# Performance work log

Hardware: AMD Instinct MI355X
Metric: run time of the kernel (lower is better)

## Reference

```python
import jax, jax.numpy as jnp
import numpy as np

B = 2
D = 256
NH = 8
DH = D // NH
L = 4
K = 2                       # sampling grid per box side
NP = K * K                  # sampled points per level
FF = 1024
NQ = 300
NE = 6
ND = 6
REF_SIZE = 4.0
SHAPES = ((64, 64), (32, 32), (16, 16), (8, 8))
S = sum(h * w for h, w in SHAPES)


def make_ref_windows():
    ws = []
    for (H, W) in SHAPES:
        y = (jnp.arange(1, H + 1, dtype=jnp.float32) - 0.5) / (H + 1e-6)
        x = (jnp.arange(1, W + 1, dtype=jnp.float32) - 0.5) / (W + 1e-6)
        yy, xx = jnp.meshgrid(y, x, indexing='ij')
        ctr = jnp.stack([xx, yy], -1).reshape(-1, 2)
        size = jnp.broadcast_to(jnp.array([REF_SIZE / W, REF_SIZE / H], jnp.float32), ctr.shape)
        ws.append(jnp.concatenate([ctr, size], -1))
    return jnp.broadcast_to(jnp.concatenate(ws, 0)[None], (B, S, 4))


def layernorm(x, g, b):
    m = jnp.mean(x, -1, keepdims=True)
    v = jnp.mean((x - m) ** 2, -1, keepdims=True)
    return (x - m) / jnp.sqrt(v + 1e-5) * g + b


def inverse_sigmoid(x, eps=1e-5):
    x = jnp.clip(x, eps, 1.0 - eps)
    return jnp.log(x / (1.0 - x))


def bilinear_sample(vl, pts, Hl, Wl):
    # vl: [B, Hl*Wl, NH, DH], pts: [B, N, NP, 2] normalized to [0,1]
    x = pts[..., 0] * Wl - 0.5
    y = pts[..., 1] * Hl - 0.5
    x0f = jnp.floor(x); y0f = jnp.floor(y)
    wx = x - x0f; wy = y - y0f
    x0 = x0f.astype(jnp.int32); y0 = y0f.astype(jnp.int32)
    Bn, N, P = x.shape

    def gather(yi, xi):
        valid = ((xi >= 0) & (xi < Wl) & (yi >= 0) & (yi < Hl)).astype(vl.dtype)
        idx = jnp.clip(yi, 0, Hl - 1) * Wl + jnp.clip(xi, 0, Wl - 1)
        g = jnp.take_along_axis(vl, idx.reshape(Bn, N * P, 1, 1), axis=1)
        return g.reshape(Bn, N, P, NH, DH) * valid[..., None, None]

    w00 = ((1 - wx) * (1 - wy))[..., None, None]
    w01 = (wx * (1 - wy))[..., None, None]
    w10 = ((1 - wx) * wy)[..., None, None]
    w11 = (wx * wy)[..., None, None]
    return (gather(y0, x0) * w00 + gather(y0, x0 + 1) * w01
            + gather(y0 + 1, x0) * w10 + gather(y0 + 1, x0 + 1) * w11)


def box_attention(q, memory, ref_windows, Wv, bv, Wa, ba, Wo, bo):
    # q: [B,N,D], memory: [B,S,D], ref_windows: [B,N,4] (cx,cy,w,h)
    Bn, N, _ = q.shape
    v = (memory @ Wv + bv).reshape(Bn, memory.shape[1], NH, DH)
    attn = jax.nn.softmax((q @ Wa + ba).reshape(Bn, N, NH, L * NP), axis=-1)
    g = (jnp.arange(K, dtype=jnp.float32) + 0.5) / K - 0.5   # grid fractions in box
    gy, gx = jnp.meshgrid(g, g, indexing='ij')
    grid = jnp.stack([gx.ravel(), gy.ravel()], -1)           # [NP,2]
    pts = ref_windows[:, :, None, :2] + grid[None, None] * ref_windows[:, :, None, 2:]
    out = jnp.zeros((Bn, N, NH, DH), q.dtype)
    start = 0
    for l, (Hl, Wl) in enumerate(SHAPES):
        sl = Hl * Wl
        sampled = bilinear_sample(v[:, start:start + sl], pts, Hl, Wl)  # [B,N,NP,NH,DH]
        out = out + jnp.einsum('bnphd,bnhp->bnhd', sampled, attn[..., l * NP:(l + 1) * NP])
        start += sl
    return out.reshape(Bn, N, D) @ Wo + bo


def mha(q_in, k_in, v_in, Wqkv, bqkv, Wo, bo):
    Bn, N, _ = q_in.shape
    q = (q_in @ Wqkv[:, :D] + bqkv[:D]).reshape(Bn, N, NH, DH)
    k = (k_in @ Wqkv[:, D:2 * D] + bqkv[D:2 * D]).reshape(Bn, N, NH, DH)
    v = (v_in @ Wqkv[:, 2 * D:] + bqkv[2 * D:]).reshape(Bn, N, NH, DH)
    a = jax.nn.softmax(jnp.einsum('bqhd,bkhd->bhqk', q, k) / jnp.sqrt(jnp.float32(DH)), axis=-1)
    o = jnp.einsum('bhqk,bkhd->bqhd', a, v).reshape(Bn, N, D)
    return o @ Wo + bo


def pos_embed_2d(coords):
    # coords: [B,N,2] -> [B,N,D] sine embedding (deformable-DETR style)
    npf = D // 2
    dim_t = 10000.0 ** (2.0 * (jnp.arange(npf) // 2) / npf)
    p = coords[..., None] * (2 * np.pi) / dim_t               # [B,N,2,npf]
    p = jnp.stack([jnp.sin(p[..., 0::2]), jnp.cos(p[..., 1::2])], -1)
    return p.reshape(coords.shape[0], coords.shape[1], 2 * npf)


def reference(src, pos, eWv, ebv, eWa, eba, eWo, ebo, eW1, eb1, eW2, eb2,
              en1g, en1b, en2g, en2b,
              dWqkv, dbqkv, dWso, dbso, dWv, dbv, dWa, dba, dWo, dbo,
              dW1, db1, dW2, db2, dn1g, dn1b, dn2g, dn2b, dn3g, dn3b,
              cls_w, cls_b, bb_w1, bb_b1, bb_w2, bb_b2, bb_w3, bb_b3,
              el_w, el_b, el_g, el_beta):
    ref_windows = make_ref_windows()
    out = src
    for i in range(NE):
        a = box_attention(out + pos, out, ref_windows, eWv[i], ebv[i], eWa[i], eba[i], eWo[i], ebo[i])
        out = layernorm(out + a, en1g[i], en1b[i])
        f = jax.nn.relu(out @ eW1[i] + eb1[i]) @ eW2[i] + eb2[i]
        out = layernorm(out + f, en2g[i], en2b[i])
    # proposal selection (topk + gather)
    valid = jnp.all((ref_windows[..., :2] > 0.01) & (ref_windows[..., :2] < 0.99), axis=-1)
    logits = (out @ cls_w + cls_b)[..., 0]
    logits = jnp.where(valid, logits, -65504.0)
    _, idx = jax.lax.top_k(logits, NQ)
    q_emb = jnp.take_along_axis(out, idx[..., None], axis=1)
    tgt = layernorm(jax.lax.stop_gradient(q_emb) @ el_w + el_b, el_g, el_beta)
    ref_sel = jnp.take_along_axis(ref_windows, idx[..., None], axis=1)
    h = jax.nn.relu(q_emb @ bb_w1 + bb_b1)
    h = jax.nn.relu(h @ bb_w2 + bb_b2)
    tmp = h @ bb_w3 + bb_b3 + inverse_sigmoid(ref_sel)
    out_ref = jax.lax.stop_gradient(jax.nn.sigmoid(tmp))
    query_pos = pos_embed_2d(out_ref[..., :2]) + pos_embed_2d(out_ref[..., 2:])
    # decoder
    x = tgt
    inter = []
    for i in range(ND):
        qk = x + query_pos
        sa = mha(qk, qk, x, dWqkv[i], dbqkv[i], dWso[i], dbso[i])
        x = layernorm(x + sa, dn1g[i], dn1b[i])
        ca = box_attention(x + query_pos, out, out_ref, dWv[i], dbv[i], dWa[i], dba[i], dWo[i], dbo[i])
        x = layernorm(x + ca, dn2g[i], dn2b[i])
        f = jax.nn.relu(x @ dW1[i] + db1[i]) @ dW2[i] + db2[i]
        x = layernorm(x + f, dn3g[i], dn3b[i])
        inter.append(x)
    return jnp.stack(inter)  # [ND, B, NQ, D]


def setup_inputs() -> dict:
    key = jax.random.key(0)
    kit = iter(jax.random.split(key, 80))
    def rn(shape, s=0.02):
        return jax.random.normal(next(kit), shape, jnp.float32) * s
    z = lambda *sh: jnp.zeros(sh, jnp.float32)
    o = lambda *sh: jnp.ones(sh, jnp.float32)
    A = NH * L * NP
    return dict(
        src=jax.random.normal(next(kit), (B, S, D), jnp.float32),
        pos=jax.random.normal(next(kit), (B, S, D), jnp.float32),
        eWv=rn((NE, D, D)), ebv=z(NE, D), eWa=rn((NE, D, A)), eba=z(NE, A),
        eWo=rn((NE, D, D)), ebo=z(NE, D),
        eW1=rn((NE, D, FF)), eb1=z(NE, FF), eW2=rn((NE, FF, D)), eb2=z(NE, D),
        en1g=o(NE, D), en1b=z(NE, D), en2g=o(NE, D), en2b=z(NE, D),
        dWqkv=rn((ND, D, 3 * D)), dbqkv=z(ND, 3 * D),
        dWso=rn((ND, D, D)), dbso=z(ND, D),
        dWv=rn((ND, D, D)), dbv=z(ND, D), dWa=rn((ND, D, A)), dba=z(ND, A),
        dWo=rn((ND, D, D)), dbo=z(ND, D),
        dW1=rn((ND, D, FF)), db1=z(ND, FF), dW2=rn((ND, FF, D)), db2=z(ND, D),
        dn1g=o(ND, D), dn1b=z(ND, D), dn2g=o(ND, D), dn2b=z(ND, D), dn3g=o(ND, D), dn3b=z(ND, D),
        cls_w=rn((D, 1)), cls_b=z(1),
        bb_w1=rn((D, D)), bb_b1=z(D), bb_w2=rn((D, D)), bb_b2=z(D),
        bb_w3=rn((D, 4)), bb_b3=z(4),
        el_w=rn((D, D)), el_b=z(D), el_g=o(D), el_beta=z(D),
    )
```

## Files before the change

### kernel.cpp

```cpp
#include <hip/hip_runtime.h>
#include <hip/hip_bf16.h>
#include <math.h>

typedef unsigned short u16;
typedef unsigned int u32;
typedef unsigned long long u64;

#define Bc   2
#define NHc  8
#define Sc   5440
#define NQc  300
#define NEc  6
#define NDc  6
#define FFc  1024
#define BSc  (Bc*Sc)
#define BNQc (Bc*NQc)

__device__ __forceinline__ float us2f(u16 u) {
    union { float f; unsigned v; } x; x.v = ((unsigned)u) << 16; return x.f;
}

__device__ __forceinline__ u16 f2bf(float f) {
    unsigned u = __float_as_uint(f);
    unsigned r = u + 0x7FFFu + ((u >> 16) & 1u);
    return (u16)(r >> 16);
}
__device__ __forceinline__ float bf2f(u16 u) { return us2f(u); }
__device__ __forceinline__ unsigned pk2(u16 a, u16 b) { return (unsigned)a | ((unsigned)b << 16); }

__device__ __forceinline__ size_t pidx(int row, int k) {
    return (size_t)(k >> 5) * ((size_t)BSc * 32) + ((size_t)row << 5) + (size_t)(k & 31);
}

__device__ __forceinline__ int xcd_swz(int orig, int nwg) {
    int xcd = orig & 7;
    int q = nwg >> 3, r = nwg & 7;
    int base = (xcd < r) ? xcd * (q + 1) : r * (q + 1) + (xcd - r) * q;
    return base + (orig >> 3);
}

using bf16x8 = __attribute__((ext_vector_type(8))) short;
using f32x4  = __attribute__((ext_vector_type(4))) float;

__global__ void k_detect(const u16* __restrict__ src, int* __restrict__ flag) {
    __shared__ int cnt;
    if (threadIdx.x == 0) cnt = 0;
    __syncthreads();
    u16 v = src[threadIdx.x];
    int e = (v >> 7) & 0xFF;
    int plaus = (e == 0) || (e >= 107 && e <= 131);
    atomicAdd(&cnt, plaus);
    __syncthreads();
    if (threadIdx.x == 0) *flag = (cnt >= 224) ? 1 : 0;
}

struct CvtArgs {
    const void* in[48];
    long off[48];
    int n[48];
    int cnt;
    long total;
};
__global__ void k_cvt_all8(CvtArgs args, float* __restrict__ out,
                           const int* __restrict__ flag) {
    long g = ((long)blockIdx.x * 256 + threadIdx.x) * 8;
    if (g >= args.total) return;
    int lo = 0, hi = args.cnt - 1;
    while (lo < hi) {
        int mid = (lo + hi + 1) >> 1;
        if (args.off[mid] <= g) lo = mid; else hi = mid - 1;
    }
    long local = g - args.off[lo];
    long n = (long)args.n[lo];
    float v[8];
#pragma unroll
    for (int j = 0; j < 8; ++j) v[j] = 0.f;
    if (*flag) {
        const u16* p = (const u16*)args.in[lo] + local;
        if (local + 8 <= n) {
            uint4 r = *(const uint4*)p;
            const u16* pu = (const u16*)&r;
#pragma unroll
            for (int j = 0; j < 8; ++j) v[j] = us2f(pu[j]);
        } else {
            for (int j = 0; j < 8; ++j)
                if (local + j < n) v[j] = us2f(p[j]);
        }
    } else {
        const float* p = (const float*)args.in[lo] + local;
        if (local + 8 <= n) {
            float4 a = ((const float4*)p)[0];
            float4 b = ((const float4*)p)[1];
            v[0] = a.x; v[1] = a.y; v[2] = a.z; v[3] = a.w;
            v[4] = b.x; v[5] = b.y; v[6] = b.z; v[7] = b.w;
        } else {
            for (int j = 0; j < 8; ++j)
                if (local + j < n) v[j] = p[j];
        }
    }
    float4 o0, o1;
    o0.x = v[0]; o0.y = v[1]; o0.z = v[2]; o0.w = v[3];
    o1.x = v[4]; o1.y = v[5]; o1.z = v[6]; o1.w = v[7];
    ((float4*)(out + g))[0] = o0;
    ((float4*)(out + g))[1] = o1;
}

__global__ void k_addf2(const float* __restrict__ a, const float* __restrict__ pos,
                        u16* __restrict__ ah, u16* __restrict__ al,
                        u16* __restrict__ ph, u16* __restrict__ pl, int n) {
    int i = blockIdx.x * 256 + threadIdx.x;
    if (i >= n) return;
    int row = i >> 8, k = i & 255;
    size_t px = pidx(row, k);
    float x = a[i];
    u16 h = f2bf(x);
    ah[px] = h;
    al[px] = f2bf(x - bf2f(h));
    float s = x + pos[i];
    u16 h2 = f2bf(s);
    ph[px] = h2;
    pl[px] = f2bf(s - bf2f(h2));
}

template<int RELU>
__global__ __launch_bounds__(256) void k_mgemm(
    const u16* __restrict__ Ah, const u16* __restrict__ Al,
    const float* __restrict__ W, const u16* __restrict__ Wraw, int ldw,
    const float* __restrict__ bias,
    float* __restrict__ C, u16* __restrict__ Ch, u16* __restrict__ Cl,
    int ldc, int K,
    const int* __restrict__ flag) {
    __shared__ __align__(16) u16 lsAH[4096];
    __shared__ __align__(16) u16 lsAL[4096];
    __shared__ __align__(16) u16 lsBH[4096];
    __shared__ __align__(16) u16 lsBL[4096];
    const int t = threadIdx.x;
    int lin = blockIdx.x + gridDim.x * blockIdx.y;
    lin = xcd_swz(lin, gridDim.x * gridDim.y);
    const int row0 = (lin / gridDim.x) * 128, col0 = (lin % gridDim.x) * 128;
    const int fast = *flag;
    const size_t PSLAB = (size_t)BSc * 32;

    const int c0 = t, c1 = 256 + t;
    const size_t abase = (size_t)row0 * 32;
    const u16* a0h = Ah + abase + (size_t)c0 * 8;
    const u16* a1h = Ah + abase + (size_t)c1 * 8;
    const u16* a0l = Al + abase + (size_t)c0 * 8;
    const u16* a1l = Al + abase + (size_t)c1 * 8;
    const unsigned d0 = (((unsigned)c0 & ~3u) | (((unsigned)c0 & 3u) ^ (((unsigned)c0 >> 3) & 3u))) * 8u;
    const unsigned d1 = (((unsigned)c1 & ~3u) | (((unsigned)c1 & 3u) ^ (((unsigned)c1 >> 3) & 3u))) * 8u;

    const int bkp = t >> 4, bno = t & 15;
    const float* bp = W + (size_t)(bkp * 2) * ldw + col0 + bno * 8;
    const u16*  brp = Wraw + (size_t)(bkp * 2) * ldw + col0 + bno * 8;

    const int lane = t & 63;
    const int w = t >> 6;
    const int wr = (w >> 1) * 64, wc = (w & 1) * 64;
    const int kg = lane >> 4, lr = lane & 15;

    unsigned iaf[4];
#pragma unroll
    for (int mi = 0; mi < 4; ++mi) {
        int arow = wr + mi * 16 + lr;
        iaf[mi] = ((unsigned)(arow << 2) + ((unsigned)kg ^ (((unsigned)arow >> 1) & 3u))) * 8u;
    }

    f32x4 acc[4][4] = {};
    uint4 aU0h, aU1h, aU0l, aU1l;
    float4 bR[4];
    uint4 bU0, bU1;
    aU0h = *(const uint4*)a0h;
    aU1h = *(const uint4*)a1h;
    aU0l = *(const uint4*)a0l;
    aU1l = *(const uint4*)a1l;
    if (fast) {
        bU0 = *(const uint4*)brp;
        bU1 = *(const uint4*)(brp + ldw);
    } else {
        const float4* q0 = (const float4*)bp;
        const float4* q1 = (const float4*)(bp + ldw);
        bR[0] = q0[0]; bR[1] = q0[1]; bR[2] = q1[0]; bR[3] = q1[1];
    }

    for (int k0 = 0; k0 < K; k0 += 32) {
        if (k0) __syncthreads();
        *(uint4*)&lsAH[d0] = aU0h;
        *(uint4*)&lsAH[d1] = aU1h;
        *(uint4*)&lsAL[d0] = aU0l;
        *(uint4*)&lsAL[d1] = aU1l;
        {
            unsigned bb = (unsigned)(bkp >> 2) * 1024u + (unsigned)(bkp & 3) * 2u;
            if (fast) {
                const u16* e0 = (const u16*)&bU0;
                const u16* e1 = (const u16*)&bU1;
#pragma unroll
                for (int j = 0; j < 8; ++j) {
                    int slot = bno * 8 + (j ^ (bno & 7));
                    *(unsigned*)&lsBH[bb + (unsigned)slot * 8u] = pk2(e0[j], e1[j]);
                }
            } else {
                float e0f[8], e1f[8];
                *(float4*)&e0f[0] = bR[0]; *(float4*)&e0f[4] = bR[1];
                *(float4*)&e1f[0] = bR[2]; *(float4*)&e1f[4] = bR[3];
#pragma unroll
                for (int j = 0; j < 8; ++j) {
                    int slot = bno * 8 + (j ^ (bno & 7));
                    u16 h0 = f2bf(e0f[j]), h1 = f2bf(e1f[j]);
                    *(unsigned*)&lsBH[bb + (unsigned)slot * 8u] = pk2(h0, h1);
                    u16 l0 = f2bf(e0f[j] - bf2f(h0));
                    u16 l1 = f2bf(e1f[j] - bf2f(h1));
                    *(unsigned*)&lsBL[bb + (unsigned)slot * 8u] = pk2(l0, l1);
                }
            }
        }
        __syncthreads();
        if (k0 + 32 < K) {
            size_t soff = (size_t)((k0 >> 5) + 1) * PSLAB;
            aU0h = *(const uint4*)(a0h + soff);
            aU1h = *(const uint4*)(a1h + soff);
            aU0l = *(const uint4*)(a0l + soff);
            aU1l = *(const uint4*)(a1l + soff);
            if (fast) {
                bU0 = *(const uint4*)(brp + (size_t)(k0 + 32) * ldw);
                bU1 = *(const uint4*)(brp + (size_t)(k0 + 33) * ldw);
            } else {
                const float4* q0 = (const float4*)(bp + (size_t)(k0 + 32) * ldw);
                const float4* q1 = (const float4*)(bp + (size_t)(k0 + 33) * ldw);
                bR[0] = q0[0]; bR[1] = q0[1]; bR[2] = q1[0]; bR[3] = q1[1];
            }
        }
        bf16x8 aH[4], aL[4], bH[4], bL[4];
#pragma unroll
        for (int mi = 0; mi < 4; ++mi) {
            aH[mi] = *(const bf16x8*)&lsAH[iaf[mi]];
            aL[mi] = *(const bf16x8*)&lsAL[iaf[mi]];
        }
#pragma unroll
        for (int ni = 0; ni < 4; ++ni) {
            int c = wc + ni * 16 + lr;
            int slot = (c & ~7) | ((c ^ (c >> 3)) & 7);
            unsigned ib = (unsigned)kg * 1024u + (unsigned)slot * 8u;
            bH[ni] = *(const bf16x8*)&lsBH[ib];
            if (!fast) bL[ni] = *(const bf16x8*)&lsBL[ib];
        }
#pragma unroll
        for (int mi = 0; mi < 4; ++mi)
#pragma unroll
            for (int ni = 0; ni < 4; ++ni) {
                acc[mi][ni] = __builtin_amdgcn_mfma_f32_16x16x32_bf16(aH[mi], bH[ni], acc[mi][ni], 0, 0, 0);
                acc[mi][ni] = __builtin_amdgcn_mfma_f32_16x16x32_bf16(aL[mi], bH[ni], acc[mi][ni], 0, 0, 0);
            }
        if (!fast) {
#pragma unroll
            for (int mi = 0; mi < 4; ++mi)
#pragma unroll
                for (int ni = 0; ni < 4; ++ni)
                    acc[mi][ni] = __builtin_amdgcn_mfma_f32_16x16x32_bf16(aH[mi], bL[ni], acc[mi][ni], 0, 0, 0);
        }
    }
    const int rb = row0 + wr + (lane >> 4) * 4;
#pragma unroll
    for (int ni = 0; ni < 4; ++ni) {
        int cc = col0 + wc + ni * 16 + lr;
        float bv = bias[cc];
#pragma unroll
        for (int mi = 0; mi < 4; ++mi) {
#pragma unroll
            for (int r2 = 0; r2 < 4; ++r2) {
                int rr = rb + mi * 16 + r2;
                float v = acc[mi][ni][r2] + bv;
                if (RELU) v = fmaxf(v, 0.f);
                if (C) C[(size_t)rr * ldc + cc] = v;
                if (Ch) {
                    size_t px = pidx(rr, cc);
                    u16 h = f2bf(v);
                    Ch[px] = h;
                    Cl[px] = f2bf(v - bf2f(h));
                }
            }
        }
    }
}

template<int RELU>
__global__ __launch_bounds__(256) void k_dgemm(
    const float* __restrict__ A, int lda,
    const float* __restrict__ W, int ldw, int wcol0,
    const float* __restrict__ bias,
    float* __restrict__ C, int ldc,
    int M, int N, int K) {
    __shared__ float As[2][16][68];
    __shared__ float Bs[2][16][68];
    int t = threadIdx.x;
    int row0 = blockIdx.y * 64, col0 = blockIdx.x * 64;
    int ti = t >> 4, tj = t & 15;
    int arow = t >> 2, akq = (t & 3) << 2;
    int bk = t >> 4, bn = (t & 15) << 2;
    bool aok = (row0 + arow) < M;
    const float* ap = A + (size_t)(row0 + arow) * lda + akq;
    const float* bp = W + (size_t)bk * ldw + wcol0 + col0 + bn;
    float4 aR = aok ? *(const float4*)ap : make_float4(0.f, 0.f, 0.f, 0.f);
    float4 bR = *(const float4*)bp;
    As[0][akq + 0][arow] = aR.x;
    As[0][akq + 1][arow] = aR.y;
    As[0][akq + 2][arow] = aR.z;
    As[0][akq + 3][arow] = aR.w;
    *(float4*)&Bs[0][bk][bn] = bR;
    __syncthreads();
    int cur = 0;
    float acc[4][4] = {};
    for (int k0 = 0; k0 < K; k0 += 16) {
        bool more = (k0 + 16) < K;
        if (more) {
            aR = aok ? *(const float4*)(ap + k0 + 16) : make_float4(0.f, 0.f, 0.f, 0.f);
            bR = *(const float4*)(bp + (size_t)(k0 + 16) * ldw);
        }
#pragma unroll
        for (int k = 0; k < 16; ++k) {
            float a[4], b[4];
#pragma unroll
            for (int r = 0; r < 4; ++r) a[r] = As[cur][k][ti * 4 + r];
#pragma unroll
            for (int c = 0; c < 4; ++c) b[c] = Bs[cur][k][tj * 4 + c];
#pragma unroll
            for (int r = 0; r < 4; ++r)
#pragma unroll
                for (int c = 0; c < 4; ++c) acc[r][c] += a[r] * b[c];
        }
        if (more) {
            int nxt = cur ^ 1;
            As[nxt][akq + 0][arow] = aR.x;
            As[nxt][akq + 1][arow] = aR.y;
            As[nxt][akq + 2][arow] = aR.z;
            As[nxt][akq + 3][arow] = aR.w;
            *(float4*)&Bs[nxt][bk][bn] = bR;
            __syncthreads();
            cur = nxt;
        }
    }
    for (int r = 0; r < 4; ++r) {
        int rr = row0 + ti * 4 + r;
        if (rr >= M) continue;
        for (int c = 0; c < 4; ++c) {
            int cc = col0 + tj * 4 + c;
            float v = acc[r][c] + bias[cc];
            if (RELU) v = fmaxf(v, 0.f);
            C[(size_t)rr * ldc + cc] = v;
        }
    }
}

__global__ __launch_bounds__(256) void k_gemm4(
    const float* __restrict__ A, const float* __restrict__ W,
    const float* __restrict__ bias, const float* __restrict__ rsel,
    float* __restrict__ oref, int M, int K) {
    int row = blockIdx.x * 64 + (threadIdx.x >> 2);
    int col = threadIdx.x & 3;
    if (row >= M) return;
    float acc = 0.f;
    const float* a = A + (size_t)row * K;
    for (int k = 0; k < K; ++k) acc += a[k] * W[k * 4 + col];
    float tmp = acc + bias[col];
    float r = rsel[(size_t)row * 4 + col];
    r = fminf(fmaxf(r, 1e-5f), 1.f - 1e-5f);
    float v = tmp + logf(r / (1.f - r));
    oref[(size_t)row * 4 + col] = 1.f / (1.f + __expf(-v));
}

__global__ void k_ln(const float* __restrict__ a, const float* __restrict__ b,
                     const float* __restrict__ g, const float* __restrict__ be,
                     float* __restrict__ o,
                     u16* __restrict__ oh, u16* __restrict__ ol,
                     const float* __restrict__ padd, float* __restrict__ opadd,
                     u16* __restrict__ oph, u16* __restrict__ opl,
                     void* __restrict__ sdst, size_t soff,
                     const int* __restrict__ flag) {
    int row = blockIdx.x;
    int t = threadIdx.x;
    __shared__ float red[256];
    size_t ix = (size_t)row * 256 + t;
    float x = a[ix];
    if (b) x += b[ix];
    red[t] = x;
    __syncthreads();
    for (int s = 128; s > 0; s >>= 1) { if (t < s) red[t] += red[t + s]; __syncthreads(); }
    float mean = red[0] / 256.f;
    __syncthreads();
    float d = x - mean;
    red[t] = d * d;
    __syncthreads();
    for (int s = 128; s > 0; s >>= 1) { if (t < s) red[t] += red[t + s]; __syncthreads(); }
    float var = red[0] / 256.f;
    float y = d * rsqrtf(var + 1e-5f) * g[t] + be[t];
    o[ix] = y;
    if (oh) {
        size_t px = pidx(row, t);
        u16 h = f2bf(y);
        oh[px] = h;
        ol[px] = f2bf(y - bf2f(h));
    }
    if (padd) {
        float z = y + padd[ix];
        if (opadd) opadd[ix] = z;
        if (oph) {
            size_t px = pidx(row, t);
            u16 h = f2bf(z);
            oph[px] = h;
            opl[px] = f2bf(z - bf2f(h));
        }
    }
    if (sdst) {
        if (*flag) ((__hip_bfloat16*)sdst)[soff + ix] = __float2bfloat16(y);
        else       ((float*)sdst)[soff + ix] = y;
    }
}

__global__ void k_refw(float* __restrict__ rw) {
    int s = blockIdx.x * 256 + threadIdx.x;
    if (s >= Sc) return;
    int start, HW;
    if (s < 4096)      { start = 0;    HW = 64; }
    else if (s < 5120) { start = 4096; HW = 32; }
    else if (s < 5376) { start = 5120; HW = 16; }
    else               { start = 5376; HW = 8;  }
    int loc = s - start;
    int i = loc / HW, j = loc % HW;
    rw[s * 4 + 0] = (j + 0.5f) / ((float)HW + 1e-6f);
    rw[s * 4 + 1] = (i + 0.5f) / ((float)HW + 1e-6f);
    rw[s * 4 + 2] = 4.0f / (float)HW;
    rw[s * 4 + 3] = 4.0f / (float)HW;
}

__global__ __launch_bounds__(256) void k_box_sample4(
    const float* __restrict__ v, const float* __restrict__ attn,
    const float* __restrict__ refw, int ref_bs,
    float* __restrict__ out, u16* __restrict__ outh, u16* __restrict__ outl,
    int N) {
    const int t = threadIdx.x;
    const int qi = t >> 6, lane = t & 63;
    const int blk = xcd_swz(blockIdx.x, gridDim.x);
    const int n = blk * 4 + qi;
    const int b = blockIdx.y;
    if (n >= N) return;
    const float* arow = attn + ((size_t)b * N + n) * 128;
    float2 wl = *(const float2*)(arow + lane * 2);
    float m = fmaxf(wl.x, wl.y);
#pragma unroll
    for (int d2 = 1; d2 < 8; d2 <<= 1) m = fmaxf(m, __shfl_xor(m, d2, 8));
    float e0 = __expf(wl.x - m), e1 = __expf(wl.y - m);
    float s = e0 + e1;
#pragma unroll
    for (int d2 = 1; d2 < 8; d2 <<= 1) s += __shfl_xor(s, d2, 8);
    float inv = 1.f / s;
    e0 *= inv; e1 *= inv;

    const float* rw = refw + (size_t)ref_bs * b + (size_t)n * 4;
    float cx = rw[0], cy = rw[1], bw = rw[2], bh = rw[3];
    const float* vb = v + (size_t)b * Sc * 256 + lane * 4;
    float4 acc = make_float4(0.f, 0.f, 0.f, 0.f);
    int start = 0;
    const int HWs[4] = {64, 32, 16, 8};
#pragma unroll
    for (int l = 0; l < 4; ++l) {
        int HW = HWs[l];
#pragma unroll
        for (int p = 0; p < 4; ++p) {
            float gx = (p & 1) ? 0.25f : -0.25f;
            float gy = (p >> 1) ? 0.25f : -0.25f;
            float x = (cx + gx * bw) * (float)HW - 0.5f;
            float y = (cy + gy * bh) * (float)HW - 0.5f;
            float x0f = floorf(x), y0f = floorf(y);
            float wx = x - x0f, wy = y - y0f;
            int x0 = (int)x0f, y0 = (int)y0f;
            float4 smp = make_float4(0.f, 0.f, 0.f, 0.f);
            if (x0 >= 0 && x0 < HW && y0 >= 0 && y0 < HW) {
                float4 g4 = *(const float4*)(vb + (size_t)(start + y0 * HW + x0) * 256);
                float wgt = (1.f - wx) * (1.f - wy);
                smp.x += wgt * g4.x; smp.y += wgt * g4.y; smp.z += wgt * g4.z; smp.w += wgt * g4.w;
            }
            if (x0 + 1 >= 0 && x0 + 1 < HW && y0 >= 0 && y0 < HW) {
                float4 g4 = *(const float4*)(vb + (size_t)(start + y0 * HW + x0 + 1) * 256);
                float wgt = wx * (1.f - wy);
                smp.x += wgt * g4.x; smp.y += wgt * g4.y; smp.z += wgt * g4.z; smp.w += wgt * g4.w;
            }
            if (x0 >= 0 && x0 < HW && y0 + 1 >= 0 && y0 + 1 < HW) {
                float4 g4 = *(const float4*)(vb + (size_t)(start + (y0 + 1) * HW + x0) * 256);
                float wgt = (1.f - wx) * wy;
                smp.x += wgt * g4.x; smp.y += wgt * g4.y; smp.z += wgt * g4.z; smp.w += wgt * g4.w;
            }
            if (x0 + 1 >= 0 && x0 + 1 < HW && y0 + 1 >= 0 && y0 + 1 < HW) {
                float4 g4 = *(const float4*)(vb + (size_t)(start + (y0 + 1) * HW + x0 + 1) * 256);
                float wgt = wx * wy;
                smp.x += wgt * g4.x; smp.y += wgt * g4.y; smp.z += wgt * g4.z; smp.w += wgt * g4.w;
            }
            const int idx = l * 4 + p;
            float wsel = (idx & 1) ? e1 : e0;
            float wv = __shfl(wsel, (lane & ~7) | (idx >> 1), 64);
            acc.x += wv * smp.x; acc.y += wv * smp.y;
            acc.z += wv * smp.z; acc.w += wv * smp.w;
        }
        start += HW * HW;
    }
    if (out) {
        size_t obase = ((size_t)b * N + n) * 256 + lane * 4;
        *(float4*)(out + obase) = acc;
    }
    if (outh) {
        size_t px = pidx(b * N + n, lane * 4);
        ushort4 h, lo;
        h.x = f2bf(acc.x); h.y = f2bf(acc.y); h.z = f2bf(acc.z); h.w = f2bf(acc.w);
        lo.x = f2bf(acc.x - bf2f(h.x)); lo.y = f2bf(acc.y - bf2f(h.y));
        lo.z = f2bf(acc.z - bf2f(h.z)); lo.w = f2bf(acc.w - bf2f(h.w));
        *(ushort4*)(outh + px) = h;
        *(ushort4*)(outl + px) = lo;
    }
}

__global__ void k_cls(const float* __restrict__ x, const float* __restrict__ w,
                      const float* __restrict__ cb, const float* __restrict__ rw,
                      float* __restrict__ logits) {
    int row = blockIdx.x;
    int t = threadIdx.x;
    __shared__ float red[256];
    red[t] = x[(size_t)row * 256 + t] * w[t];
    __syncthreads();
    for (int s = 128; s > 0; s >>= 1) { if (t < s) red[t] += red[t + s]; __syncthreads(); }
    if (t == 0) {
        int s = row % Sc;
        float cx = rw[s * 4], cy = rw[s * 4 + 1];
        bool valid = (cx > 0.01f) && (cx < 0.99f) && (cy > 0.01f) && (cy < 0.99f);
        logits[row] = valid ? (red[0] + cb[0]) : -65504.0f;
    }
}

__global__ void k_topk(const float* __restrict__ logits, int* __restrict__ idxout) {
    int b = blockIdx.x;
    int t = threadIdx.x;
    __shared__ unsigned keys[Sc];
    __shared__ int hist[256];
    __shared__ int suf[257];
    __shared__ unsigned sprefix;
    __shared__ int sR;
    __shared__ int cnt;
    __shared__ u64 cand[512];
    for (int i = t; i < Sc; i += 256) {
        union { float f; unsigned u; } x;
        x.f = logits[(size_t)b * Sc + i];
        unsigned u = x.u;
        keys[i] = (u & 0x80000000u) ? ~u : (u | 0x80000000u);
    }
    if (t == 0) { sprefix = 0; sR = NQc; suf[256] = 0; }
    __syncthreads();
    for (int shift = 24; shift >= 0; shift -= 8) {
        hist[t] = 0;
        __syncthreads();
        unsigned pref = sprefix;
        int R = sR;
        unsigned pmask = (shift == 24) ? 0u : (0xFFFFFFFFu << (shift + 8));
        for (int i = t; i < Sc; i += 256) {
            unsigned kk = keys[i];
            if ((kk & pmask) == (pref & pmask))
                atomicAdd(&hist[(kk >> shift) & 255], 1);
        }
        __syncthreads();
        suf[t] = hist[t];
        __syncthreads();
        for (int s2 = 1; s2 < 256; s2 <<= 1) {
            int vv = suf[t] + ((t + s2 < 256) ? suf[t + s2] : 0);
            __syncthreads();
            suf[t] = vv;
            __syncthreads();
        }
        if (suf[t] >= R && suf[t + 1] < R) {
            sR = R - suf[t + 1];
            sprefix = pref | ((unsigned)t << shift);
        }
        __syncthreads();
    }
    unsigned T = sprefix;
    if (t == 0) cnt = 0;
    __syncthreads();
    for (int i = t; i < Sc; i += 256) {
        unsigned kk = keys[i];
        if (kk >= T) {
            int slot = atomicAdd(&cnt, 1);
            if (slot < 512)
                cand[slot] = ~((((u64)kk) << 32) | (u64)(0xFFFFFFFFu - (unsigned)i));
        }
    }
    __syncthreads();
    int total = cnt < 512 ? cnt : 512;
    for (int i = t; i < 512; i += 256)
        if (i >= total) cand[i] = 0xFFFFFFFFFFFFFFFFull;
    __syncthreads();
    for (int i = t; i < 512; i += 256) {
        if (i >= total) continue;
        u64 mine = cand[i];
        int rank = 0;
        for (int j = 0; j < 512; ++j) rank += (cand[j] < mine) ? 1 : 0;
        if (rank < NQc) {
            u64 c = ~mine;
            idxout[b * NQc + rank] = (int)(0xFFFFFFFFu - (unsigned)(c & 0xFFFFFFFFull));
        }
    }
}

__global__ void k_gather(const float* __restrict__ x, const float* __restrict__ rw,
                         const int* __restrict__ idx, float* __restrict__ qemb,
                         float* __restrict__ refsel) {
    int q = blockIdx.x, b = blockIdx.y;
    int t = threadIdx.x;
    int id = idx[b * NQc + q];
    qemb[((size_t)b * NQc + q) * 256 + t] = x[((size_t)b * Sc + id) * 256 + t];
    if (t < 4) refsel[((size_t)b * NQc + q) * 4 + t] = rw[id * 4 + t];
}

__global__ void k_qpos(const float* __restrict__ outref, float* __restrict__ qpos) {
    int n = blockIdx.x, b = blockIdx.y;
    int t = threadIdx.x;
    const float* orf = outref + ((size_t)b * NQc + n) * 4;
    int c = t >> 7;
    int j = (t & 127) >> 1;
    int si = t & 1;
    float tj = powf(10000.f, (float)j / 64.f);
    float sc = 6.283185307179586f / tj;
    float v1 = orf[c] * sc;
    float v2 = orf[2 + c] * sc;
    float r = si ? (cosf(v1) + cosf(v2)) : (sinf(v1) + sinf(v2));
    qpos[((size_t)b * NQc + n) * 256 + t] = r;
}

#define NSPL 10
#define SPLW 30
__global__ __launch_bounds__(256) void k_mha2(
    const float* __restrict__ qk, const float* __restrict__ v,
    float* __restrict__ opart, float* __restrict__ mlpart) {
    __shared__ float lsK[SPLW][256];
    __shared__ float lsV[SPLW][256];
    const int t = threadIdx.x;
    const int h = t >> 5, ql = t & 31;
    const int b = blockIdx.y, z = blockIdx.z;
    const int n = blockIdx.x * 32 + ql;
    const bool qok = n < NQc;
    const int kstart = z * SPLW;
    for (int f = t; f < SPLW * 64; f += 256) {
        int r = f >> 6, c4 = f & 63;
        int krow = kstart + r;
        float4 kv = *(const float4*)(qk + (size_t)(b * NQc + krow) * 512 + 256 + c4 * 4);
        float4 vv = *(const float4*)(v + (size_t)(b * NQc + krow) * 256 + c4 * 4);
        *(float4*)&lsK[r][c4 * 4] = kv;
        *(float4*)&lsV[r][c4 * 4] = vv;
    }
    __syncthreads();
    float q[32];
    {
        const float* qp = qk + (size_t)(b * NQc + (qok ? n : 0)) * 512 + h * 32;
#pragma unroll
        for (int j4 = 0; j4 < 8; ++j4) {
            float4 f = ((const float4*)qp)[j4];
            q[j4 * 4 + 0] = f.x; q[j4 * 4 + 1] = f.y;
            q[j4 * 4 + 2] = f.z; q[j4 * 4 + 3] = f.w;
        }
    }
    const float scale = 0.17677669529663688f;
    float s[SPLW];
#pragma unroll
    for (int kk = 0; kk < SPLW; ++kk) {
        float acc = 0.f;
        const float* kr = &lsK[kk][h * 32];
#pragma unroll
        for (int j4 = 0; j4 < 8; ++j4) {
            float4 kf = ((const float4*)kr)[j4];
            acc += q[j4*4+0]*kf.x + q[j4*4+1]*kf.y + q[j4*4+2]*kf.z + q[j4*4+3]*kf.w;
        }
        s[kk] = acc * scale;
    }
    float m = s[0];
#pragma unroll
    for (int kk = 1; kk < SPLW; ++kk) m = fmaxf(m, s[kk]);
    float o[32];
#pragma unroll
    for (int j = 0; j < 32; ++j) o[j] = 0.f;
    float l = 0.f;
#pragma unroll
    for (int kk = 0; kk < SPLW; ++kk) {
        float e = __expf(s[kk] - m);
        l += e;
        const float* vr = &lsV[kk][h * 32];
#pragma unroll
        for (int j4 = 0; j4 < 8; ++j4) {
            float4 vf = ((const float4*)vr)[j4];
            o[j4*4+0] += e * vf.x; o[j4*4+1] += e * vf.y;
            o[j4*4+2] += e * vf.z; o[j4*4+3] += e * vf.w;
        }
    }
    if (qok) {
        float* op = opart + ((size_t)z * BNQc + (size_t)b * NQc + n) * 256 + h * 32;
#pragma unroll
        for (int j4 = 0; j4 < 8; ++j4) {
            float4 f;
            f.x = o[j4*4+0]; f.y = o[j4*4+1]; f.z = o[j4*4+2]; f.w = o[j4*4+3];
            ((float4*)op)[j4] = f;
        }
        float* mlp = mlpart + ((size_t)z * BNQc + (size_t)b * NQc + n) * 16 + h * 2;
        mlp[0] = m; mlp[1] = l;
    }
}

__global__ void k_mha_comb(const float* __restrict__ opart, const float* __restrict__ mlpart,
                           float* __restrict__ out) {
    int row = blockIdx.x;
    int t = threadIdx.x;
    int h = t >> 5;
    float mm[NSPL], ll[NSPL];
    float M = -3.0e38f;
#pragma unroll
    for (int z = 0; z < NSPL; ++z) {
        mm[z] = mlpart[((size_t)z * BNQc + row) * 16 + h * 2];
        ll[z] = mlpart[((size_t)z * BNQc + row) * 16 + h * 2 + 1];
        M = fmaxf(M, mm[z]);
    }
    float denom = 0.f, osum = 0.f;
#pragma unroll
    for (int z = 0; z < NSPL; ++z) {
        float a = __expf(mm[z] - M);
        denom += ll[z] * a;
        osum += opart[((size_t)z * BNQc + row) * 256 + t] * a;
    }
    out[(size_t)row * 256 + t] = osum / denom;
}

extern "C" void kernel_launch(void* const* d_in, const int* in_sizes, int n_in,
                              void* d_out, int out_size, void* d_ws, size_t ws_size,
                              hipStream_t stream) {
    char* base = (char*)d_ws;
    size_t off = 0;
    auto allocB = [&](size_t bytes) {
        char* p = base + off;
        off = (off + bytes + 255) & ~(size_t)255;
        return p;
    };
    int* flag = (int*)allocB(16);
    auto allocF = [&](size_t n) { return (float*)allocB(n * 4); };
    auto allocH = [&](size_t n) { return (u16*)allocB(n * 2); };

    k_detect<<<1, 256, 0, stream>>>((const u16*)d_in[0], flag);

    CvtArgs ca;
    long acc = 0;
    int ninp = n_in < 48 ? n_in : 48;
    for (int i = 0; i < 48; ++i) {
        int idx2 = i < ninp ? i : ninp - 1;
        ca.in[i] = d_in[idx2];
        ca.n[i] = (i < ninp) ? in_sizes[i] : 0;
        ca.off[i] = acc;
        acc += ((long)ca.n[i] + 63) & ~63L;
    }
    ca.cnt = 48;
    ca.total = acc;
    float* cvtbase = allocF((size_t)acc);
    k_cvt_all8<<<(int)((acc / 8 + 255) / 256), 256, 0, stream>>>(ca, cvtbase, flag);
    float* F[48];
    for (int i = 0; i < 48; ++i) F[i] = cvtbase + ca.off[i];

    const size_t BSD = (size_t)BSc * 256;
    float* enc    = F[0];
    u16* encH  = allocH(BSD);  u16* encL  = allocH(BSD);
    u16* pbufH = allocH(BSD);  u16* pbufL = allocH(BSD);
    u16* tbufH = allocH(BSD);  u16* tbufL = allocH(BSD);
    u16* ffnhH = allocH((size_t)BSc * FFc);
    u16* ffnhL = allocH((size_t)BSc * FFc);
    float* vbuf   = allocF(BSD);
    float* gout   = allocF(BSD);
    float* attnb  = allocF((size_t)BSc * 128);
    float* refw   = allocF(Sc * 4);
    float* logit  = allocF(BSc);
    int*   idx    = (int*)allocB(BNQc * 4);
    float* qemb   = allocF((size_t)BNQc * 256);
    float* rsel   = allocF(BNQc * 4);
    float* xbuf   = allocF((size_t)BNQc * 256);
    float* qposb  = allocF((size_t)BNQc * 256);
    float* dqk    = allocF((size_t)BNQc * 256);
    float* dqk512 = allocF((size_t)BNQc * 512);
    float* dv     = allocF((size_t)BNQc * 256);
    float* dt1    = allocF((size_t)BNQc * 256);
    float* dt2    = allocF((size_t)BNQc * 256);
    float* datt   = allocF((size_t)BNQc * 128);
    float* dffnh  = allocF((size_t)BNQc * FFc);
    float* h1f    = allocF((size_t)BNQc * 256);
    float* h2f    = allocF((size_t)BNQc * 256);
    float* oref   = allocF(BNQc * 4);
    float* opart  = allocF((size_t)NSPL * BNQc * 256);
    float* mlpart = allocF((size_t)NSPL * BNQc * 16);
    (void)ws_size; (void)out_size;

    auto MG = [&](int relu, const u16* Ah, const u16* Al, int widx, size_t woff, int ldw,
                  const float* bias, float* Cf, u16* Ch, u16* Cl, int ldc, int N, int K) {
        const float* Wf = F[widx] + woff;
        const u16* Wraw = (const u16*)d_in[widx] + woff;
        dim3 g(N / 128, BSc / 128);
        if (relu) k_mgemm<1><<<g, 256, 0, stream>>>(Ah, Al, Wf, Wraw, ldw, bias, Cf, Ch, Cl, ldc, K, flag);
        else      k_mgemm<0><<<g, 256, 0, stream>>>(Ah, Al, Wf, Wraw, ldw, bias, Cf, Ch, Cl, ldc, K, flag);
    };
    auto DG = [&](int relu, const float* A, int lda, const float* W, int ldw, int wcol0,
                  const float* bias, float* C, int ldc, int M, int N, int K) {
        dim3 g(N / 64, (M + 63) / 64);
        if (relu) k_dgemm<1><<<g, 256, 0, stream>>>(A, lda, W, ldw, wcol0, bias, C, ldc, M, N, K);
        else      k_dgemm<0><<<g, 256, 0, stream>>>(A, lda, W, ldw, wcol0, bias, C, ldc, M, N, K);
    };

    const int nBSD = (int)BSD;
    k_refw<<<(Sc + 255) / 256, 256, 0, stream>>>(refw);
    k_addf2<<<(nBSD + 255) / 256, 256, 0, stream>>>(enc, F[1], encH, encL, pbufH, pbufL, nBSD);

    for (int i = 0; i < NEc; ++i) {
        MG(0, encH, encL, 2, (size_t)i * 65536, 256, F[3] + i * 256, vbuf, nullptr, nullptr, 256, 256, 256);
        MG(0, pbufH, pbufL, 4, (size_t)i * 32768, 128, F[5] + i * 128, attnb, nullptr, nullptr, 128, 128, 256);
        k_box_sample4<<<dim3((Sc + 3) / 4, Bc), 256, 0, stream>>>(vbuf, attnb, refw, 0,
                                                                  nullptr, tbufH, tbufL, Sc);
        MG(0, tbufH, tbufL, 6, (size_t)i * 65536, 256, F[7] + i * 256, gout, nullptr, nullptr, 256, 256, 256);
        k_ln<<<BSc, 256, 0, stream>>>(enc, gout, F[12] + i * 256, F[13] + i * 256,
                                      enc, encH, encL,
                                      nullptr, nullptr, nullptr, nullptr,
                                      nullptr, 0, flag);
        MG(1, encH, encL, 8, (size_t)i * 262144, 1024, F[9] + i * 1024,
           nullptr, ffnhH, ffnhL, 1024, 1024, 256);
        MG(0, ffnhH, ffnhL, 10, (size_t)i * 262144, 256, F[11] + i * 256,
           gout, nullptr, nullptr, 256, 256, 1024);
        k_ln<<<BSc, 256, 0, stream>>>(enc, gout, F[14] + i * 256, F[15] + i * 256,
                                      enc, encH, encL,
                                      (i < NEc - 1) ? F[1] : nullptr, nullptr,
                                      (i < NEc - 1) ? pbufH : nullptr,
                                      (i < NEc - 1) ? pbufL : nullptr,
                                      nullptr, 0, flag);
    }

    k_cls<<<BSc, 256, 0, stream>>>(enc, F[36], F[37], refw, logit);
    k_topk<<<Bc, 256, 0, stream>>>(logit, idx);
    k_gather<<<dim3(NQc, Bc), 256, 0, stream>>>(enc, refw, idx, qemb, rsel);
    DG(0, qemb, 256, F[44], 256, 0, F[45], dt1, 256, BNQc, 256, 256);
    DG(1, qemb, 256, F[38], 256, 0, F[39], h1f, 256, BNQc, 256, 256);
    DG(1, h1f,  256, F[40], 256, 0, F[41], h2f, 256, BNQc, 256, 256);
    k_gemm4<<<(BNQc + 63) / 64, 256, 0, stream>>>(h2f, F[42], F[43], rsel, oref, BNQc, 256);
    k_qpos<<<dim3(NQc, Bc), 256, 0, stream>>>(oref, qposb);
    k_ln<<<BNQc, 256, 0, stream>>>(dt1, nullptr, F[46], F[47],
                                   xbuf, nullptr, nullptr,
                                   qposb, dqk, nullptr, nullptr,
                                   nullptr, 0, flag);

    const int nXD = BNQc * 256;
    for (int i = 0; i < NDc; ++i) {
        DG(0, dqk,  256, F[16] + (size_t)i * 196608, 768, 0,   F[17] + i * 768,       dqk512, 512, BNQc, 512, 256);
        DG(0, xbuf, 256, F[16] + (size_t)i * 196608, 768, 512, F[17] + i * 768 + 512, dv,     256, BNQc, 256, 256);
        k_mha2<<<dim3((NQc + 31) / 32, Bc, NSPL), 256, 0, stream>>>(dqk512, dv, opart, mlpart);
        k_mha_comb<<<BNQc, 256, 0, stream>>>(opart, mlpart, dt1);
        DG(0, dt1, 256, F[18] + (size_t)i * 65536, 256, 0, F[19] + i * 256, dt2, 256, BNQc, 256, 256);
        k_ln<<<BNQc, 256, 0, stream>>>(xbuf, dt2, F[30] + i * 256, F[31] + i * 256,
                                       xbuf, nullptr, nullptr,
                                       qposb, dqk, nullptr, nullptr,
                                       nullptr, 0, flag);
        MG(0, encH, encL, 20, (size_t)i * 65536, 256, F[21] + i * 256, vbuf, nullptr, nullptr, 256, 256, 256);
        DG(0, dqk, 256, F[22] + (size_t)i * 32768, 128, 0, F[23] + i * 128, datt, 128, BNQc, 128, 256);
        k_box_sample4<<<dim3((NQc + 3) / 4, Bc), 256, 0, stream>>>(vbuf, datt, oref, NQc * 4,
                                                                   dt1, nullptr, nullptr, NQc);
        DG(0, dt1, 256, F[24] + (size_t)i * 65536, 256, 0, F[25] + i * 256, dt2, 256, BNQc, 256, 256);
        k_ln<<<BNQc, 256, 0, stream>>>(xbuf, dt2, F[32] + i * 256, F[33] + i * 256,
                                       xbuf, nullptr, nullptr,
                                       nullptr, nullptr, nullptr, nullptr,
                                       nullptr, 0, flag);
        DG(1, xbuf,  256,  F[26] + (size_t)i * 262144, 1024, 0, F[27] + i * 1024, dffnh, 1024, BNQc, 1024, 256);
        DG(0, dffnh, 1024, F[28] + (size_t)i * 262144, 256,  0, F[29] + i * 256,  dt2,   256,  BNQc, 256, 1024);
        k_ln<<<BNQc, 256, 0, stream>>>(xbuf, dt2, F[34] + i * 256, F[35] + i * 256,
                                       xbuf, nullptr, nullptr,
                                       (i < NDc - 1) ? qposb : nullptr,
                                       (i < NDc - 1) ? dqk : nullptr, nullptr, nullptr,
                                       d_out, (size_t)i * nXD, flag);
    }
}
```

Measured before the change: 2.808 ms.

## Prefetch two K-slabs ahead in GEMM and skip converting unused bf16 weights

```diff
diff --git a/kernel.cpp b/kernel.cpp
--- a/kernel.cpp
+++ b/kernel.cpp
@@ -60,6 +60,7 @@
     int n[48];
     int cnt;
     long total;
+    u64 skip;
 };
 __global__ void k_cvt_all8(CvtArgs args, float* __restrict__ out,
                            const int* __restrict__ flag) {
@@ -76,6 +77,7 @@
 #pragma unroll
     for (int j = 0; j < 8; ++j) v[j] = 0.f;
     if (*flag) {
+        if ((args.skip >> lo) & 1) return;
         const u16* p = (const u16*)args.in[lo] + local;
         if (local + 8 <= n) {
             uint4 r = *(const uint4*)p;
@@ -153,6 +155,7 @@
     const int bkp = t >> 4, bno = t & 15;
     const float* bp = W + (size_t)(bkp * 2) * ldw + col0 + bno * 8;
     const u16*  brp = Wraw + (size_t)(bkp * 2) * ldw + col0 + bno * 8;
+    const unsigned bb = (unsigned)(bkp >> 2) * 1024u + (unsigned)(bkp & 3) * 2u;
 
     const int lane = t & 63;
     const int w = t >> 6;
@@ -167,69 +170,66 @@
     }
 
     f32x4 acc[4][4] = {};
-    uint4 aU0h, aU1h, aU0l, aU1l;
-    float4 bR[4];
-    uint4 bU0, bU1;
-    aU0h = *(const uint4*)a0h;
-    aU1h = *(const uint4*)a1h;
-    aU0l = *(const uint4*)a0l;
-    aU1l = *(const uint4*)a1l;
-    if (fast) {
-        bU0 = *(const uint4*)brp;
-        bU1 = *(const uint4*)(brp + ldw);
-    } else {
-        const float4* q0 = (const float4*)bp;
-        const float4* q1 = (const float4*)(bp + ldw);
-        bR[0] = q0[0]; bR[1] = q0[1]; bR[2] = q1[0]; bR[3] = q1[1];
-    }
-
-    for (int k0 = 0; k0 < K; k0 += 32) {
-        if (k0) __syncthreads();
-        *(uint4*)&lsAH[d0] = aU0h;
-        *(uint4*)&lsAH[d1] = aU1h;
-        *(uint4*)&lsAL[d0] = aU0l;
-        *(uint4*)&lsAL[d1] = aU1l;
-        {
-            unsigned bb = (unsigned)(bkp >> 2) * 1024u + (unsigned)(bkp & 3) * 2u;
-            if (fast) {
-                const u16* e0 = (const u16*)&bU0;
-                const u16* e1 = (const u16*)&bU1;
-#pragma unroll
-                for (int j = 0; j < 8; ++j) {
-                    int slot = bno * 8 + (j ^ (bno & 7));
-                    *(unsigned*)&lsBH[bb + (unsigned)slot * 8u] = pk2(e0[j], e1[j]);
-                }
-            } else {
-                float e0f[8], e1f[8];
-                *(float4*)&e0f[0] = bR[0]; *(float4*)&e0f[4] = bR[1];
-                *(float4*)&e1f[0] = bR[2]; *(float4*)&e1f[4] = bR[3];
-#pragma unroll
-                for (int j = 0; j < 8; ++j) {
-                    int slot = bno * 8 + (j ^ (bno & 7));
-                    u16 h0 = f2bf(e0f[j]), h1 = f2bf(e1f[j]);
-                    *(unsigned*)&lsBH[bb + (unsigned)slot * 8u] = pk2(h0, h1);
-                    u16 l0 = f2bf(e0f[j] - bf2f(h0));
-                    u16 l1 = f2bf(e1f[j] - bf2f(h1));
-                    *(unsigned*)&lsBL[bb + (unsigned)slot * 8u] = pk2(l0, l1);
-                }
+
+    uint4 A0h0, A0h1, A0l0, A0l1, A1h0, A1h1, A1l0, A1l1;
+    uint4 bUa0, bUa1, bUb0, bUb1;
+    float4 bRa[4], bRb[4];
+
+    auto loadA0 = [&](int slab) {
+        size_t so = (size_t)slab * PSLAB;
+        A0h0 = *(const uint4*)(a0h + so); A0h1 = *(const uint4*)(a1h + so);
+        A0l0 = *(const uint4*)(a0l + so); A0l1 = *(const uint4*)(a1l + so);
+    };
+    auto loadA1 = [&](int slab) {
+        size_t so = (size_t)slab * PSLAB;
+        A1h0 = *(const uint4*)(a0h + so); A1h1 = *(const uint4*)(a1h + so);
+        A1l0 = *(const uint4*)(a0l + so); A1l1 = *(const uint4*)(a1l + so);
+    };
+    auto loadBa = [&](int k) {
+        if (fast) {
+            bUa0 = *(const uint4*)(brp + (size_t)k * ldw);
+            bUa1 = *(const uint4*)(brp + (size_t)(k + 1) * ldw);
+        } else {
+            const float4* q0 = (const float4*)(bp + (size_t)k * ldw);
+            const float4* q1 = (const float4*)(bp + (size_t)(k + 1) * ldw);
+            bRa[0] = q0[0]; bRa[1] = q0[1]; bRa[2] = q1[0]; bRa[3] = q1[1];
+        }
+    };
+    auto loadBb = [&](int k) {
+        if (fast) {
+            bUb0 = *(const uint4*)(brp + (size_t)k * ldw);
+            bUb1 = *(const uint4*)(brp + (size_t)(k + 1) * ldw);
+        } else {
+            const float4* q0 = (const float4*)(bp + (size_t)k * ldw);
+            const float4* q1 = (const float4*)(bp + (size_t)(k + 1) * ldw);
+            bRb[0] = q0[0]; bRb[1] = q0[1]; bRb[2] = q1[0]; bRb[3] = q1[1];
+        }
+    };
+    auto stageB = [&](const uint4& u0, const uint4& u1, const float4* br) {
+        if (fast) {
+            const u16* e0 = (const u16*)&u0;
+            const u16* e1 = (const u16*)&u1;
+#pragma unroll
+            for (int j = 0; j < 8; ++j) {
+                int slot = bno * 8 + (j ^ (bno & 7));
+                *(unsigned*)&lsBH[bb + (unsigned)slot * 8u] = pk2(e0[j], e1[j]);
             }
-        }
-        __syncthreads();
-        if (k0 + 32 < K) {
-            size_t soff = (size_t)((k0 >> 5) + 1) * PSLAB;
-            aU0h = *(const uint4*)(a0h + soff);
-            aU1h = *(const uint4*)(a1h + soff);
-            aU0l = *(const uint4*)(a0l + soff);
-            aU1l = *(const uint4*)(a1l + soff);
-            if (fast) {
-                bU0 = *(const uint4*)(brp + (size_t)(k0 + 32) * ldw);
-                bU1 = *(const uint4*)(brp + (size_t)(k0 + 33) * ldw);
-            } else {
-                const float4* q0 = (const float4*)(bp + (size_t)(k0 + 32) * ldw);
-                const float4* q1 = (const float4*)(bp + (size_t)(k0 + 33) * ldw);
-                bR[0] = q0[0]; bR[1] = q0[1]; bR[2] = q1[0]; bR[3] = q1[1];
+        } else {
+            float e0f[8], e1f[8];
+            *(float4*)&e0f[0] = br[0]; *(float4*)&e0f[4] = br[1];
+            *(float4*)&e1f[0] = br[2]; *(float4*)&e1f[4] = br[3];
+#pragma unroll
+            for (int j = 0; j < 8; ++j) {
+                int slot = bno * 8 + (j ^ (bno & 7));
+                u16 h0 = f2bf(e0f[j]), h1 = f2bf(e1f[j]);
+                *(unsigned*)&lsBH[bb + (unsigned)slot * 8u] = pk2(h0, h1);
+                u16 l0 = f2bf(e0f[j] - bf2f(h0));
+                u16 l1 = f2bf(e1f[j] - bf2f(h1));
+                *(unsigned*)&lsBL[bb + (unsigned)slot * 8u] = pk2(l0, l1);
             }
         }
+    };
+    auto compute = [&]() {
         bf16x8 aH[4], aL[4], bH[4], bL[4];
 #pragma unroll
         for (int mi = 0; mi < 4; ++mi) {
@@ -258,7 +258,32 @@
                 for (int ni = 0; ni < 4; ++ni)
                     acc[mi][ni] = __builtin_amdgcn_mfma_f32_16x16x32_bf16(aH[mi], bL[ni], acc[mi][ni], 0, 0, 0);
         }
-    }
+    };
+
+    loadA0(0); loadBa(0);
+    loadA1(1); loadBb(32);
+
+    for (int k0 = 0; k0 < K; k0 += 64) {
+        if (k0) __syncthreads();
+        *(uint4*)&lsAH[d0] = A0h0;
+        *(uint4*)&lsAH[d1] = A0h1;
+        *(uint4*)&lsAL[d0] = A0l0;
+        *(uint4*)&lsAL[d1] = A0l1;
+        stageB(bUa0, bUa1, bRa);
+        __syncthreads();
+        if (k0 + 64 < K) { loadA0((k0 >> 5) + 2); loadBa(k0 + 64); }
+        compute();
+        __syncthreads();
+        *(uint4*)&lsAH[d0] = A1h0;
+        *(uint4*)&lsAH[d1] = A1h1;
+        *(uint4*)&lsAL[d0] = A1l0;
+        *(uint4*)&lsAL[d1] = A1l1;
+        stageB(bUb0, bUb1, bRb);
+        __syncthreads();
+        if (k0 + 96 < K) { loadA1((k0 >> 5) + 3); loadBb(k0 + 96); }
+        compute();
+    }
+
     const int rb = row0 + wr + (lane >> 4) * 4;
 #pragma unroll
     for (int ni = 0; ni < 4; ++ni) {
@@ -759,6 +784,8 @@
     }
     ca.cnt = 48;
     ca.total = acc;
+    ca.skip = (1ull << 2) | (1ull << 4) | (1ull << 6) | (1ull << 8) |
+              (1ull << 10) | (1ull << 20);
     float* cvtbase = allocF((size_t)acc);
     k_cvt_all8<<<(int)((acc / 8 + 255) / 256), 256, 0, stream>>>(ca, cvtbase, flag);
     float* F[48];
```

Measured after the change: 2.923 ms. 4.1% more time.

## Batch six decoder value projections into one z-batched GEMM and skip unused weight conversions

Applied to the files above, without the earlier changes.

```diff
diff --git a/kernel.cpp b/kernel.cpp
--- a/kernel.cpp
+++ b/kernel.cpp
@@ -60,6 +60,7 @@
     int n[48];
     int cnt;
     long total;
+    u64 skip;
 };
 __global__ void k_cvt_all8(CvtArgs args, float* __restrict__ out,
                            const int* __restrict__ flag) {
@@ -76,6 +77,7 @@
 #pragma unroll
     for (int j = 0; j < 8; ++j) v[j] = 0.f;
     if (*flag) {
+        if ((args.skip >> lo) & 1) return;
         const u16* p = (const u16*)args.in[lo] + local;
         if (local + 8 <= n) {
             uint4 r = *(const uint4*)p;
@@ -126,8 +128,10 @@
 __global__ __launch_bounds__(256) void k_mgemm(
     const u16* __restrict__ Ah, const u16* __restrict__ Al,
     const float* __restrict__ W, const u16* __restrict__ Wraw, int ldw,
-    const float* __restrict__ bias,
-    float* __restrict__ C, u16* __restrict__ Ch, u16* __restrict__ Cl,
+    size_t wstride,
+    const float* __restrict__ bias, int bstride,
+    float* __restrict__ C, size_t cstride,
+    u16* __restrict__ Ch, u16* __restrict__ Cl,
     int ldc, int K,
     const int* __restrict__ flag) {
     __shared__ __align__(16) u16 lsAH[4096];
@@ -138,8 +142,13 @@
     int lin = blockIdx.x + gridDim.x * blockIdx.y;
     lin = xcd_swz(lin, gridDim.x * gridDim.y);
     const int row0 = (lin / gridDim.x) * 128, col0 = (lin % gridDim.x) * 128;
+    const int z = blockIdx.z;
     const int fast = *flag;
     const size_t PSLAB = (size_t)BSc * 32;
+    W += (size_t)z * wstride;
+    Wraw += (size_t)z * wstride;
+    C += (size_t)z * cstride;
+    bias += (size_t)z * bstride;
 
     const int c0 = t, c1 = 256 + t;
     const size_t abase = (size_t)row0 * 32;
@@ -759,6 +768,8 @@
     }
     ca.cnt = 48;
     ca.total = acc;
+    ca.skip = (1ull << 2) | (1ull << 4) | (1ull << 6) | (1ull << 8) |
+              (1ull << 10) | (1ull << 20);
     float* cvtbase = allocF((size_t)acc);
     k_cvt_all8<<<(int)((acc / 8 + 255) / 256), 256, 0, stream>>>(ca, cvtbase, flag);
     float* F[48];
@@ -772,6 +783,7 @@
     u16* ffnhH = allocH((size_t)BSc * FFc);
     u16* ffnhL = allocH((size_t)BSc * FFc);
     float* vbuf   = allocF(BSD);
+    float* vbuf6  = allocF((size_t)NDc * BSD);
     float* gout   = allocF(BSD);
     float* attnb  = allocF((size_t)BSc * 128);
     float* refw   = allocF(Sc * 4);
@@ -796,12 +808,15 @@
     (void)ws_size; (void)out_size;
 
     auto MG = [&](int relu, const u16* Ah, const u16* Al, int widx, size_t woff, int ldw,
-                  const float* bias, float* Cf, u16* Ch, u16* Cl, int ldc, int N, int K) {
+                  const float* bias, float* Cf, u16* Ch, u16* Cl, int ldc, int N, int K,
+                  int nz, size_t wstride, int bstride, size_t cstride) {
         const float* Wf = F[widx] + woff;
         const u16* Wraw = (const u16*)d_in[widx] + woff;
-        dim3 g(N / 128, BSc / 128);
-        if (relu) k_mgemm<1><<<g, 256, 0, stream>>>(Ah, Al, Wf, Wraw, ldw, bias, Cf, Ch, Cl, ldc, K, flag);
-        else      k_mgemm<0><<<g, 256, 0, stream>>>(Ah, Al, Wf, Wraw, ldw, bias, Cf, Ch, Cl, ldc, K, flag);
+        dim3 g(N / 128, BSc / 128, nz);
+        if (relu) k_mgemm<1><<<g, 256, 0, stream>>>(Ah, Al, Wf, Wraw, ldw, wstride,
+                                                    bias, bstride, Cf, cstride, Ch, Cl, ldc, K, flag);
+        else      k_mgemm<0><<<g, 256, 0, stream>>>(Ah, Al, Wf, Wraw, ldw, wstride,
+                                                    bias, bstride, Cf, cstride, Ch, Cl, ldc, K, flag);
     };
     auto DG = [&](int relu, const float* A, int lda, const float* W, int ldw, int wcol0,
                   const float* bias, float* C, int ldc, int M, int N, int K) {
@@ -815,19 +830,22 @@
     k_addf2<<<(nBSD + 255) / 256, 256, 0, stream>>>(enc, F[1], encH, encL, pbufH, pbufL, nBSD);
 
     for (int i = 0; i < NEc; ++i) {
-        MG(0, encH, encL, 2, (size_t)i * 65536, 256, F[3] + i * 256, vbuf, nullptr, nullptr, 256, 256, 256);
-        MG(0, pbufH, pbufL, 4, (size_t)i * 32768, 128, F[5] + i * 128, attnb, nullptr, nullptr, 128, 128, 256);
+        MG(0, encH, encL, 2, (size_t)i * 65536, 256, F[3] + i * 256, vbuf, nullptr, nullptr,
+           256, 256, 256, 1, 0, 0, 0);
+        MG(0, pbufH, pbufL, 4, (size_t)i * 32768, 128, F[5] + i * 128, attnb, nullptr, nullptr,
+           128, 128, 256, 1, 0, 0, 0);
         k_box_sample4<<<dim3((Sc + 3) / 4, Bc), 256, 0, stream>>>(vbuf, attnb, refw, 0,
                                                                   nullptr, tbufH, tbufL, Sc);
-        MG(0, tbufH, tbufL, 6, (size_t)i * 65536, 256, F[7] + i * 256, gout, nullptr, nullptr, 256, 256, 256);
+        MG(0, tbufH, tbufL, 6, (size_t)i * 65536, 256, F[7] + i * 256, gout, nullptr, nullptr,
+           256, 256, 256, 1, 0, 0, 0);
         k_ln<<<BSc, 256, 0, stream>>>(enc, gout, F[12] + i * 256, F[13] + i * 256,
                                       enc, encH, encL,
                                       nullptr, nullptr, nullptr, nullptr,
                                       nullptr, 0, flag);
         MG(1, encH, encL, 8, (size_t)i * 262144, 1024, F[9] + i * 1024,
-           nullptr, ffnhH, ffnhL, 1024, 1024, 256);
+           nullptr, ffnhH, ffnhL, 1024, 1024, 256, 1, 0, 0, 0);
         MG(0, ffnhH, ffnhL, 10, (size_t)i * 262144, 256, F[11] + i * 256,
-           gout, nullptr, nullptr, 256, 256, 1024);
+           gout, nullptr, nullptr, 256, 256, 1024, 1, 0, 0, 0);
         k_ln<<<BSc, 256, 0, stream>>>(enc, gout, F[14] + i * 256, F[15] + i * 256,
                                       enc, encH, encL,
                                       (i < NEc - 1) ? F[1] : nullptr, nullptr,
@@ -839,6 +857,8 @@
     k_cls<<<BSc, 256, 0, stream>>>(enc, F[36], F[37], refw, logit);
     k_topk<<<Bc, 256, 0, stream>>>(logit, idx);
     k_gather<<<dim3(NQc, Bc), 256, 0, stream>>>(enc, refw, idx, qemb, rsel);
+    MG(0, encH, encL, 20, 0, 256, F[21], vbuf6, nullptr, nullptr,
+       256, 256, 256, NDc, 65536, 256, BSD);
     DG(0, qemb, 256, F[44], 256, 0, F[45], dt1, 256, BNQc, 256, 256);
     DG(1, qemb, 256, F[38], 256, 0, F[39], h1f, 256, BNQc, 256, 256);
     DG(1, h1f,  256, F[40], 256, 0, F[41], h2f, 256, BNQc, 256, 256);
@@ -860,9 +880,9 @@
                                        xbuf, nullptr, nullptr,
                                        qposb, dqk, nullptr, nullptr,
                                        nullptr, 0, flag);
-        MG(0, encH, encL, 20, (size_t)i * 65536, 256, F[21] + i * 256, vbuf, nullptr, nullptr, 256, 256, 256);
         DG(0, dqk, 256, F[22] + (size_t)i * 32768, 128, 0, F[23] + i * 128, datt, 128, BNQc, 128, 256);
-        k_box_sample4<<<dim3((NQc + 3) / 4, Bc), 256, 0, stream>>>(vbuf, datt, oref, NQc * 4,
+        k_box_sample4<<<dim3((NQc + 3) / 4, Bc), 256, 0, stream>>>(vbuf6 + (size_t)i * BSD, datt,
+                                                                   oref, NQc * 4,
                                                                    dt1, nullptr, nullptr, NQc);
         DG(0, dt1, 256, F[24] + (size_t)i * 65536, 256, 0, F[25] + i * 256, dt2, 256, BNQc, 256, 256);
         k_ln<<<BNQc, 256, 0, stream>>>(xbuf, dt2, F[32] + i * 256, F[33] + i * 256,
```

After: 2.737 ms (median of 2 runs). -2.5%, faster.
